# Kernel optimization log

Hardware: AMD Instinct MI355X
Metric: run time of the kernel (lower is better)

Reference implementation:

```python
import jax, jax.numpy as jnp
import numpy as np

N_NODES = 100000
N_EDGES = 1600000
HEADS = 4
HID = 32
NEG_SLOPE = 0.2
EPS = 1e-16


def _gat_layer(x, w, a_src, a_dst, b, src, dst, n_nodes, concat):
    # x: [N, F_in], w: [H*C, F_in], a_src/a_dst: [H, C]
    H, C = a_src.shape
    h = (x @ w.T).reshape(-1, H, C)                      # [N, H, C]
    alpha_src = jnp.einsum('nhc,hc->nh', h, a_src)       # [N, H]
    alpha_dst = jnp.einsum('nhc,hc->nh', h, a_dst)       # [N, H]
    e = alpha_src[src] + alpha_dst[dst]                  # [E, H]
    e = jax.nn.leaky_relu(e, NEG_SLOPE)
    # segment softmax over incoming edges of each dst node
    m = jax.ops.segment_max(e, dst, num_segments=n_nodes)   # [N, H]
    ex = jnp.exp(e - m[dst])
    denom = jax.ops.segment_sum(ex, dst, num_segments=n_nodes)  # [N, H]
    alpha = ex / (denom[dst] + EPS)                      # [E, H]
    msg = alpha[:, :, None] * h[src]                     # [E, H, C]
    out = jax.ops.segment_sum(msg, dst, num_segments=n_nodes)  # [N, H, C]
    if concat:
        out = out.reshape(n_nodes, H * C)
    else:
        out = out.mean(axis=1)
    return out + b


def setup_inputs() -> dict:
    key = jax.random.key(0)
    ks = jax.random.split(key, 16)
    x = jax.random.normal(ks[0], (N_NODES, 3), dtype=jnp.float32)
    edge_index = jax.random.randint(ks[1], (2, N_EDGES), 0, N_NODES, dtype=jnp.int64 if jax.config.read('jax_enable_x64') else jnp.int32)
    s = 0.1
    return {
        'x': x,
        'edge_index': edge_index,
        'w1': jax.random.normal(ks[2], (HEADS * HID, 3)) * s,
        'att_src1': jax.random.normal(ks[3], (HEADS, HID)) * s,
        'att_dst1': jax.random.normal(ks[4], (HEADS, HID)) * s,
        'b1': jax.random.normal(ks[5], (HEADS * HID,)) * s,
        'w2': jax.random.normal(ks[6], (HID, HEADS * HID)) * s,
        'att_src2': jax.random.normal(ks[7], (1, HID)) * s,
        'att_dst2': jax.random.normal(ks[8], (1, HID)) * s,
        'b2': jax.random.normal(ks[9], (HID,)) * s,
        'mlp_w1': jax.random.normal(ks[10], (HID, 2 * HID)) * s,
        'mlp_b1': jax.random.normal(ks[11], (HID,)) * s,
        'mlp_w2': jax.random.normal(ks[12], (1, HID)) * s,
        'mlp_b2': jax.random.normal(ks[13], (1,)) * s,
    }


def reference(x, edge_index, w1, att_src1, att_dst1, b1, w2, att_src2, att_dst2, b2,
              mlp_w1, mlp_b1, mlp_w2, mlp_b2):
    src, dst = edge_index[0], edge_index[1]
    n = x.shape[0]
    # dropout layers are identity in eval mode
    h = _gat_layer(x, w1, att_src1, att_dst1, b1, src, dst, n, concat=True)   # [N, H*C]
    h = jax.nn.elu(h)
    h = _gat_layer(h, w2, att_src2, att_dst2, b2, src, dst, n, concat=False)  # [N, C]
    ef = jnp.concatenate([h[src], h[dst]], axis=-1)                            # [E, 2C]
    ef = jax.nn.relu(ef @ mlp_w1.T + mlp_b1)
    flows = (ef @ mlp_w2.T + mlp_b2).squeeze(-1)                               # [E]
    return jax.nn.relu(flows)
```

## Files before the change

### kernel.cpp

```cpp
#include <hip/hip_runtime.h>
#include <hip/hip_fp16.h>
#include <math.h>

#define N_NODES 100000
#define N_EDGES 1600000
#define NEG_SLOPE 0.2f
#define EPS 1e-16f

#define NBUCK 196
#define CHUNK 4096
#define BLKB 391

typedef _Float16 f16x8 __attribute__((ext_vector_type(8)));
typedef float f32x4 __attribute__((ext_vector_type(4)));

__device__ __forceinline__ float lrelu(float v) { return v > 0.f ? v : NEG_SLOPE * v; }

__device__ __forceinline__ float4 ld4h(const __half* p) {
    uint2 r = *(const uint2*)p;
    __half2 h0 = *reinterpret_cast<const __half2*>(&r.x);
    __half2 h1 = *reinterpret_cast<const __half2*>(&r.y);
    float2 f0 = __half22float2(h0), f1 = __half22float2(h1);
    return make_float4(f0.x, f0.y, f1.x, f1.y);
}

__device__ __forceinline__ void ld8h(const __half* p, float* f) {
    uint4 r = *(const uint4*)p;
    __half2 h0 = *reinterpret_cast<const __half2*>(&r.x);
    __half2 h1 = *reinterpret_cast<const __half2*>(&r.y);
    __half2 h2 = *reinterpret_cast<const __half2*>(&r.z);
    __half2 h3 = *reinterpret_cast<const __half2*>(&r.w);
    float2 f0 = __half22float2(h0), f1 = __half22float2(h1);
    float2 f2 = __half22float2(h2), f3 = __half22float2(h3);
    f[0] = f0.x; f[1] = f0.y; f[2] = f1.x; f[3] = f1.y;
    f[4] = f2.x; f[5] = f2.y; f[6] = f3.x; f[7] = f3.y;
}

__global__ void kA_hist(const int* __restrict__ ei, int* __restrict__ bh) {
    __shared__ int hist[NBUCK];
    int tid = threadIdx.x, b = blockIdx.x;
    if (tid < NBUCK) hist[tid] = 0;
    __syncthreads();
    int base = b * CHUNK;
    #pragma unroll
    for (int i = 0; i < CHUNK / 256; i++) {
        int e = base + i * 256 + tid;
        if (e < N_EDGES) {
            int dst = ei[N_EDGES + e];
            atomicAdd(&hist[dst >> 9], 1);
        }
    }
    __syncthreads();
    if (tid < NBUCK) bh[b * NBUCK + tid] = hist[tid];
}

__global__ void kS1(int* __restrict__ bh, int* __restrict__ bucketStart) {
    __shared__ int tsum[256];
    int k = blockIdx.x, t = threadIdx.x;
    int j0 = 2 * t, j1 = 2 * t + 1;
    int v0 = (j0 < BLKB) ? bh[j0 * NBUCK + k] : 0;
    int v1 = (j1 < BLKB) ? bh[j1 * NBUCK + k] : 0;
    int s = v0 + v1;
    tsum[t] = s;
    __syncthreads();
    for (int off = 1; off < 256; off <<= 1) {
        int tv = (t >= off) ? tsum[t - off] : 0;
        __syncthreads();
        tsum[t] += tv;
        __syncthreads();
    }
    int excl = tsum[t] - s;
    if (j0 < BLKB) bh[j0 * NBUCK + k] = excl;
    if (j1 < BLKB) bh[j1 * NBUCK + k] = excl + v0;
    if (t == 255) bucketStart[k] = tsum[255];
}

__global__ void kS2(int* __restrict__ bucketStart) {
    __shared__ int tmp[256];
    int t = threadIdx.x;
    int v = (t < NBUCK) ? bucketStart[t] : 0;
    tmp[t] = v;
    __syncthreads();
    for (int off = 1; off < 256; off <<= 1) {
        int tv = (t >= off) ? tmp[t - off] : 0;
        __syncthreads();
        tmp[t] += tv;
        __syncthreads();
    }
    if (t < NBUCK) bucketStart[t] = tmp[t] - v;
    if (t == NBUCK - 1) bucketStart[NBUCK] = tmp[t];
}

__global__ void kB_bin(const int* __restrict__ ei, const int* __restrict__ bh,
                       const int* __restrict__ bucketStart, int* __restrict__ binned) {
    __shared__ int cur[NBUCK];
    int tid = threadIdx.x, b = blockIdx.x;
    if (tid < NBUCK) cur[tid] = bucketStart[tid] + bh[b * NBUCK + tid];
    __syncthreads();
    int base = b * CHUNK;
    #pragma unroll
    for (int i = 0; i < CHUNK / 256; i++) {
        int e = base + i * 256 + tid;
        if (e < N_EDGES) {
            int src = ei[e], dst = ei[N_EDGES + e];
            int pos = atomicAdd(&cur[dst >> 9], 1);
            binned[pos] = src | ((dst & 511) << 17);
        }
    }
}

__global__ void kC_sort(const int* __restrict__ bucketStart, const int* __restrict__ binned,
                        int* __restrict__ deg, int* __restrict__ rowptr,
                        int* __restrict__ csr_src) {
    __shared__ int cnt[512];
    __shared__ int pfx[512];
    __shared__ int bsum[256];
    int t = threadIdx.x, k = blockIdx.x;
    int s0 = bucketStart[k], s1 = bucketStart[k + 1];
    cnt[t] = 0; cnt[t + 256] = 0;
    __syncthreads();
    for (int i = s0 + t; i < s1; i += 256)
        atomicAdd(&cnt[binned[i] >> 17], 1);
    __syncthreads();
    int a0 = cnt[2 * t], a1 = cnt[2 * t + 1];
    int s = a0 + a1;
    bsum[t] = s;
    __syncthreads();
    for (int off = 1; off < 256; off <<= 1) {
        int tv = (t >= off) ? bsum[t - off] : 0;
        __syncthreads();
        bsum[t] += tv;
        __syncthreads();
    }
    int excl = bsum[t] - s;
    pfx[2 * t] = excl;
    pfx[2 * t + 1] = excl + a0;
    int nb0 = k << 9;
    int n0 = nb0 + 2 * t, n1 = nb0 + 2 * t + 1;
    if (n0 < N_NODES) { deg[n0] = a0; rowptr[n0] = s0 + excl; }
    if (n1 < N_NODES) { deg[n1] = a1; rowptr[n1] = s0 + excl + a0; }
    __syncthreads();
    for (int i = s0 + t; i < s1; i += 256) {
        int pkd = binned[i];
        int pos = s0 + atomicAdd(&pfx[pkd >> 17], 1);
        csr_src[pos] = pkd & 0x1FFFF;
    }
}

__global__ void k_q(const float* __restrict__ w1, const float* __restrict__ as1,
                    const float* __restrict__ ad1, float* __restrict__ qv) {
    int t = threadIdx.x;
    if (t >= 24) return;
    int c = t % 3, h = (t / 3) % 4, side = t / 12;
    const float* att = side ? ad1 : as1;
    float acc = 0.f;
    for (int cc = 0; cc < 32; cc++)
        acc += att[h * 32 + cc] * w1[(h * 32 + cc) * 3 + c];
    qv[t] = acc;
}

__global__ void k_node1(const float* __restrict__ x, const float* __restrict__ qv,
                        float* __restrict__ a1d, __half* __restrict__ p1h) {
    int n = blockIdx.x * blockDim.x + threadIdx.x;
    if (n >= N_NODES) return;
    float x0 = x[n * 3], x1 = x[n * 3 + 1], x2 = x[n * 3 + 2];
    float s0 = x0 * qv[0]  + x1 * qv[1]  + x2 * qv[2];
    float s1 = x0 * qv[3]  + x1 * qv[4]  + x2 * qv[5];
    float s2 = x0 * qv[6]  + x1 * qv[7]  + x2 * qv[8];
    float s3 = x0 * qv[9]  + x1 * qv[10] + x2 * qv[11];
    float4 d;
    d.x = x0 * qv[12] + x1 * qv[13] + x2 * qv[14];
    d.y = x0 * qv[15] + x1 * qv[16] + x2 * qv[17];
    d.z = x0 * qv[18] + x1 * qv[19] + x2 * qv[20];
    d.w = x0 * qv[21] + x1 * qv[22] + x2 * qv[23];
    ((float4*)a1d)[n] = d;
    __half2 h0 = __floats2half2_rn(s0, s1);
    __half2 h1 = __floats2half2_rn(s2, s3);
    __half2 h2v = __floats2half2_rn(x0, x1);
    __half2 h3 = __floats2half2_rn(x2, 1.f);
    uint4 st;
    st.x = *reinterpret_cast<unsigned int*>(&h0);
    st.y = *reinterpret_cast<unsigned int*>(&h1);
    st.z = *reinterpret_cast<unsigned int*>(&h2v);
    st.w = *reinterpret_cast<unsigned int*>(&h3);
    *reinterpret_cast<uint4*>(p1h + n * 8) = st;
}

#define G1_BLOCKS ((N_NODES + 63) / 64)
__global__ void k_gat1(const int* __restrict__ rowptr, const int* __restrict__ deg,
                       const int* __restrict__ csr_src,
                       const __half* __restrict__ p1h, const float* __restrict__ w1,
                       const float* __restrict__ a1d,
                       const float* __restrict__ b1, const float* __restrict__ w2,
                       const float* __restrict__ as2, const float* __restrict__ ad2,
                       __half* __restrict__ h2, float* __restrict__ a2s, float* __restrict__ a2d) {
    __shared__ float sm[64][16];
    __shared__ __align__(16) __half F1h[4][16][136];
    int tid = threadIdx.x;
    int wave = tid >> 6, lane = tid & 63;

    int nl = wave * 16 + (lane >> 2);
    int h  = lane & 3;
    int n  = blockIdx.x * 64 + nl;
    if (n < N_NODES) {
        float4 ad4 = ((const float4*)a1d)[n];
        float adv[4] = {ad4.x, ad4.y, ad4.z, ad4.w};
        int beg = rowptr[n], cnt = deg[n];
        float acc[4][4];
        #pragma unroll
        for (int hh = 0; hh < 4; hh++)
            acc[hh][0] = acc[hh][1] = acc[hh][2] = acc[hh][3] = 0.f;
        int t = h;
        for (; t + 12 < cnt; t += 16) {
            int i0 = csr_src[beg + t],     i1 = csr_src[beg + t + 4];
            int i2 = csr_src[beg + t + 8], i3 = csr_src[beg + t + 12];
            float g0[8], g1[8], g2[8], g3[8];
            ld8h(p1h + i0 * 8, g0);
            ld8h(p1h + i1 * 8, g1);
            ld8h(p1h + i2 * 8, g2);
            ld8h(p1h + i3 * 8, g3);
            #pragma unroll
            for (int hh = 0; hh < 4; hh++) {
                float e0 = __expf(lrelu(g0[hh] + adv[hh]));
                float e1 = __expf(lrelu(g1[hh] + adv[hh]));
                float e2 = __expf(lrelu(g2[hh] + adv[hh]));
                float e3 = __expf(lrelu(g3[hh] + adv[hh]));
                acc[hh][0] += e0 * g0[4] + e1 * g1[4] + e2 * g2[4] + e3 * g3[4];
                acc[hh][1] += e0 * g0[5] + e1 * g1[5] + e2 * g2[5] + e3 * g3[5];
                acc[hh][2] += e0 * g0[6] + e1 * g1[6] + e2 * g2[6] + e3 * g3[6];
                acc[hh][3] += e0 + e1 + e2 + e3;
            }
        }
        for (; t < cnt; t += 4) {
            int i0 = csr_src[beg + t];
            float g0[8];
            ld8h(p1h + i0 * 8, g0);
            #pragma unroll
            for (int hh = 0; hh < 4; hh++) {
                float e0 = __expf(lrelu(g0[hh] + adv[hh]));
                acc[hh][0] += e0 * g0[4];
                acc[hh][1] += e0 * g0[5];
                acc[hh][2] += e0 * g0[6];
                acc[hh][3] += e0;
            }
        }
        #pragma unroll
        for (int hh = 0; hh < 4; hh++) {
            #pragma unroll
            for (int cc = 0; cc < 4; cc++) {
                float vv = acc[hh][cc];
                vv += __shfl_xor(vv, 1);
                vv += __shfl_xor(vv, 2);
                acc[hh][cc] = vv;
            }
        }
        float4 r;
        r.x = h == 0 ? acc[0][0] : h == 1 ? acc[1][0] : h == 2 ? acc[2][0] : acc[3][0];
        r.y = h == 0 ? acc[0][1] : h == 1 ? acc[1][1] : h == 2 ? acc[2][1] : acc[3][1];
        r.z = h == 0 ? acc[0][2] : h == 1 ? acc[1][2] : h == 2 ? acc[2][2] : acc[3][2];
        r.w = h == 0 ? acc[0][3] : h == 1 ? acc[1][3] : h == 2 ? acc[2][3] : acc[3][3];
        *(float4*)&sm[nl][h * 4] = r;
    }

    f16x8 Bf[2][4];
    {
        int bn = lane & 15, bg = lane >> 4;
        #pragma unroll
        for (int tile = 0; tile < 2; tile++) {
            const float* wrow = w2 + (tile * 16 + bn) * 128 + bg * 8;
            #pragma unroll
            for (int ks = 0; ks < 4; ks++) {
                const float4* wp = (const float4*)(wrow + ks * 32);
                float4 u0 = wp[0], u1 = wp[1];
                f16x8 bf;
                bf[0] = (_Float16)u0.x; bf[1] = (_Float16)u0.y;
                bf[2] = (_Float16)u0.z; bf[3] = (_Float16)u0.w;
                bf[4] = (_Float16)u1.x; bf[5] = (_Float16)u1.y;
                bf[6] = (_Float16)u1.z; bf[7] = (_Float16)u1.w;
                Bf[tile][ks] = bf;
            }
        }
    }

    int j = lane, j2 = lane + 64;
    int h0 = j >> 5;
    float wa0 = w1[j * 3], wa1 = w1[j * 3 + 1], wa2 = w1[j * 3 + 2];
    float wb0 = w1[j2 * 3], wb1 = w1[j2 * 3 + 1], wb2 = w1[j2 * 3 + 2];
    float b1j = b1[j], b1j2 = b1[j2];

    #pragma unroll 1
    for (int i = 0; i < 16; i++) {
        int n2 = blockIdx.x * 64 + wave * 16 + i;
        if (n2 >= N_NODES) break;
        const float* S = sm[wave * 16 + i];
        float v0 = (wa0 * S[h0 * 4] + wa1 * S[h0 * 4 + 1] + wa2 * S[h0 * 4 + 2])
                   / (S[h0 * 4 + 3] + EPS) + b1j;
        float v1 = (wb0 * S[(2 + h0) * 4] + wb1 * S[(2 + h0) * 4 + 1] + wb2 * S[(2 + h0) * 4 + 2])
                   / (S[(2 + h0) * 4 + 3] + EPS) + b1j2;
        float e0 = v0 > 0.f ? v0 : __expf(v0) - 1.f;
        float e1 = v1 > 0.f ? v1 : __expf(v1) - 1.f;
        F1h[wave][i][j]  = __float2half(e0);
        F1h[wave][i][j2] = __float2half(e1);
    }

    f32x4 d0 = {0.f, 0.f, 0.f, 0.f}, d1 = {0.f, 0.f, 0.f, 0.f};
    {
        int am = lane & 15, ag = lane >> 4;
        const __half* Arow = &F1h[wave][am][0];
        #pragma unroll
        for (int ks = 0; ks < 4; ks++) {
            f16x8 af = *(const f16x8*)&Arow[ks * 32 + ag * 8];
            d0 = __builtin_amdgcn_mfma_f32_16x16x32_f16(af, Bf[0][ks], d0, 0, 0, 0);
            d1 = __builtin_amdgcn_mfma_f32_16x16x32_f16(af, Bf[1][ks], d1, 0, 0, 0);
        }
    }

    {
        int ch = lane & 15, rg = lane >> 4;
        float as2a = as2[ch], as2b = as2[ch + 16];
        float ad2a = ad2[ch], ad2b = ad2[ch + 16];
        #pragma unroll
        for (int r = 0; r < 4; r++) {
            int n2 = blockIdx.x * 64 + wave * 16 + rg * 4 + r;
            float va = d0[r], vb = d1[r];
            if (n2 < N_NODES) {
                h2[n2 * 32 + ch]      = __float2half(va);
                h2[n2 * 32 + ch + 16] = __float2half(vb);
            }
            float ps = va * as2a + vb * as2b;
            float pd = va * ad2a + vb * ad2b;
            ps += __shfl_xor(ps, 1); ps += __shfl_xor(ps, 2);
            ps += __shfl_xor(ps, 4); ps += __shfl_xor(ps, 8);
            pd += __shfl_xor(pd, 1); pd += __shfl_xor(pd, 2);
            pd += __shfl_xor(pd, 4); pd += __shfl_xor(pd, 8);
            if (ch == 0 && n2 < N_NODES) { a2s[n2] = ps; a2d[n2] = pd; }
        }
    }
}

#define G2_BLOCKS ((N_NODES + 15) / 16)
__global__ void k_gat2(const int* __restrict__ rowptr, const int* __restrict__ deg,
                       const int* __restrict__ csr_src,
                       const __half* __restrict__ h2, const float* __restrict__ a2s,
                       const float* __restrict__ a2d, const float* __restrict__ b2,
                       const float* __restrict__ mw1, const float* __restrict__ mb1,
                       __half* __restrict__ u, __half* __restrict__ v) {
    __shared__ __align__(16) float WT[32][68];
    __shared__ int   pidx[4][68];
    __shared__ float pe[4][68];
    __shared__ float hfv[4][144];
    int tid = threadIdx.x;
    for (int i = tid; i < 2048; i += 256) {
        int s = i >> 5, k = i & 31;
        WT[k][s] = mw1[(s & 31) * 64 + (s >> 5) * 32 + k];
    }
    __syncthreads();
    int lane = tid & 63, w = tid >> 6;
    int nl = lane >> 4, sl = lane & 15;
    int eg2 = sl >> 2, qq = sl & 3;
    int n = blockIdx.x * 16 + w * 4 + nl;
    float4 b2a = ((const float4*)b2)[qq * 2];
    float4 b2b = ((const float4*)b2)[qq * 2 + 1];

    int beg = 0, cnt = 0;
    float ad = 0.f;
    if (n < N_NODES) { beg = rowptr[n]; cnt = deg[n]; ad = a2d[n]; }

    float acc[8] = {0.f, 0.f, 0.f, 0.f, 0.f, 0.f, 0.f, 0.f};
    float den = 0.f;
    int pkbase = nl * 17;
    for (int b16 = 0; b16 < cnt; b16 += 16) {
        int li = b16 + sl;
        int idx = (li < cnt) ? csr_src[beg + li] : 0;
        float e = 0.f;
        if (li < cnt) e = __expf(lrelu(a2s[idx] + ad));
        den += e;
        pidx[w][pkbase + sl] = idx;
        pe[w][pkbase + sl]   = e;
        #pragma unroll
        for (int p = 0; p < 4; p++) {
            int id = pidx[w][pkbase + p * 4 + eg2];
            float ee = pe[w][pkbase + p * 4 + eg2];
            float g[8];
            ld8h(h2 + id * 32 + qq * 8, g);
            acc[0] += ee * g[0]; acc[1] += ee * g[1];
            acc[2] += ee * g[2]; acc[3] += ee * g[3];
            acc[4] += ee * g[4]; acc[5] += ee * g[5];
            acc[6] += ee * g[6]; acc[7] += ee * g[7];
        }
    }
    #pragma unroll
    for (int j = 0; j < 8; j++) {
        float vv = acc[j];
        vv += __shfl_xor(vv, 4);
        vv += __shfl_xor(vv, 8);
        acc[j] = vv;
    }
    den += __shfl_xor(den, 1); den += __shfl_xor(den, 2);
    den += __shfl_xor(den, 4); den += __shfl_xor(den, 8);
    float inv = 1.f / (den + EPS);
    if (sl < 4) {
        float4 ha, hb;
        ha.x = acc[0] * inv + b2a.x; ha.y = acc[1] * inv + b2a.y;
        ha.z = acc[2] * inv + b2a.z; ha.w = acc[3] * inv + b2a.w;
        hb.x = acc[4] * inv + b2b.x; hb.y = acc[5] * inv + b2b.y;
        hb.z = acc[6] * inv + b2b.z; hb.w = acc[7] * inv + b2b.w;
        *(float4*)&hfv[w][nl * 36 + sl * 8]     = ha;
        *(float4*)&hfv[w][nl * 36 + sl * 8 + 4] = hb;
    }
    if (n < N_NODES) {
        int half_o = sl >> 3, c4 = (sl & 7) * 4;
        __half* outp = half_o ? v : u;
        float r0 = half_o ? 0.f : mb1[c4 + 0];
        float r1 = half_o ? 0.f : mb1[c4 + 1];
        float r2 = half_o ? 0.f : mb1[c4 + 2];
        float r3 = half_o ? 0.f : mb1[c4 + 3];
        const float* hfp = &hfv[w][nl * 36];
        int s4 = sl * 4;
        #pragma unroll
        for (int k = 0; k < 32; k++) {
            float hk = hfp[k];
            float4 wv = *(const float4*)&WT[k][s4];
            r0 += wv.x * hk; r1 += wv.y * hk;
            r2 += wv.z * hk; r3 += wv.w * hk;
        }
        __half2 p0, p1;
        p0.x = __float2half(r0); p0.y = __float2half(r1);
        p1.x = __float2half(r2); p1.y = __float2half(r3);
        uint2 st;
        st.x = *reinterpret_cast<unsigned int*>(&p0);
        st.y = *reinterpret_cast<unsigned int*>(&p1);
        *reinterpret_cast<uint2*>(outp + n * 32 + c4) = st;
    }
}

#define MLP_BLOCKS 4096
__global__ void k_mlp(const int* __restrict__ ei, const __half* __restrict__ u,
                      const __half* __restrict__ v, const float* __restrict__ mw2,
                      const float* __restrict__ mb2, float* __restrict__ out) {
    int tid = threadIdx.x;
    int q = tid & 7;
    float4 w2q = ((const float4*)mw2)[q];
    float mb20 = mb2[0];
    int g = blockIdx.x * 32 + (tid >> 3);
    const int stride = MLP_BLOCKS * 32 * 4;
    for (int e = g * 4; e < N_EDGES; e += stride) {
        int eb = e;
        int e1 = (eb + 1 < N_EDGES) ? eb + 1 : eb;
        int e2 = (eb + 2 < N_EDGES) ? eb + 2 : eb;
        int e3 = (eb + 3 < N_EDGES) ? eb + 3 : eb;
        int sa = ei[eb], da = ei[N_EDGES + eb];
        int sb = ei[e1], db = ei[N_EDGES + e1];
        int sc = ei[e2], dc = ei[N_EDGES + e2];
        int sd = ei[e3], dd = ei[N_EDGES + e3];
        float4 ua = ld4h(u + sa * 32 + q * 4);
        float4 va = ld4h(v + da * 32 + q * 4);
        float4 ub = ld4h(u + sb * 32 + q * 4);
        float4 vb = ld4h(v + db * 32 + q * 4);
        float4 uc = ld4h(u + sc * 32 + q * 4);
        float4 vc = ld4h(v + dc * 32 + q * 4);
        float4 ud = ld4h(u + sd * 32 + q * 4);
        float4 vd = ld4h(v + dd * 32 + q * 4);
        float s0 = fmaxf(ua.x + va.x, 0.f) * w2q.x + fmaxf(ua.y + va.y, 0.f) * w2q.y
                 + fmaxf(ua.z + va.z, 0.f) * w2q.z + fmaxf(ua.w + va.w, 0.f) * w2q.w;
        float s1 = fmaxf(ub.x + vb.x, 0.f) * w2q.x + fmaxf(ub.y + vb.y, 0.f) * w2q.y
                 + fmaxf(ub.z + vb.z, 0.f) * w2q.z + fmaxf(ub.w + vb.w, 0.f) * w2q.w;
        float s2 = fmaxf(uc.x + vc.x, 0.f) * w2q.x + fmaxf(uc.y + vc.y, 0.f) * w2q.y
                 + fmaxf(uc.z + vc.z, 0.f) * w2q.z + fmaxf(uc.w + vc.w, 0.f) * w2q.w;
        float s3 = fmaxf(ud.x + vd.x, 0.f) * w2q.x + fmaxf(ud.y + vd.y, 0.f) * w2q.y
                 + fmaxf(ud.z + vd.z, 0.f) * w2q.z + fmaxf(ud.w + vd.w, 0.f) * w2q.w;
        s0 += __shfl_xor(s0, 1, 8); s0 += __shfl_xor(s0, 2, 8); s0 += __shfl_xor(s0, 4, 8);
        s1 += __shfl_xor(s1, 1, 8); s1 += __shfl_xor(s1, 2, 8); s1 += __shfl_xor(s1, 4, 8);
        s2 += __shfl_xor(s2, 1, 8); s2 += __shfl_xor(s2, 2, 8); s2 += __shfl_xor(s2, 4, 8);
        s3 += __shfl_xor(s3, 1, 8); s3 += __shfl_xor(s3, 2, 8); s3 += __shfl_xor(s3, 4, 8);
        if (q == 0) {
            out[eb] = fmaxf(s0 + mb20, 0.f);
            if (eb + 1 < N_EDGES) out[eb + 1] = fmaxf(s1 + mb20, 0.f);
            if (eb + 2 < N_EDGES) out[eb + 2] = fmaxf(s2 + mb20, 0.f);
            if (eb + 3 < N_EDGES) out[eb + 3] = fmaxf(s3 + mb20, 0.f);
        }
    }
}

extern "C" void kernel_launch(void* const* d_in, const int* in_sizes, int n_in,
                              void* d_out, int out_size, void* d_ws, size_t ws_size,
                              hipStream_t stream) {
    const float* x    = (const float*)d_in[0];
    const int*   ei   = (const int*)d_in[1];
    const float* w1   = (const float*)d_in[2];
    const float* as1  = (const float*)d_in[3];
    const float* ad1  = (const float*)d_in[4];
    const float* b1   = (const float*)d_in[5];
    const float* w2   = (const float*)d_in[6];
    const float* as2  = (const float*)d_in[7];
    const float* ad2  = (const float*)d_in[8];
    const float* b2   = (const float*)d_in[9];
    const float* mw1  = (const float*)d_in[10];
    const float* mb1  = (const float*)d_in[11];
    const float* mw2  = (const float*)d_in[12];
    const float* mb2  = (const float*)d_in[13];
    float* out = (float*)d_out;

    const int N = N_NODES;
    char* base   = (char*)d_ws;
    int* deg     = (int*)(base);
    int* rowptr  = (int*)(base + 400000);
    int* bstart  = (int*)(base + 800000);
    int* bh      = (int*)(base + 1200000);
    int* csr_src = (int*)(base + 1602048);
    __half* p1h  = (__half*)(base + 8002048);
    float* a1d   = (float*)(base + 11202048);
    __half* h2   = (__half*)(base + 12802048);
    int* binned  = (int*)(base + 19202048);
    float* a2s   = (float*)(base + 25602048);
    float* a2d   = (float*)(base + 26002048);
    __half* u    = (__half*)(base + 26402048);
    __half* v    = (__half*)(base + 32802048);
    float* qv    = (float*)(base + 39202048);

    const int nb = (N + 255) / 256;

    kA_hist<<<BLKB, 256, 0, stream>>>(ei, bh);
    kS1<<<NBUCK, 256, 0, stream>>>(bh, bstart);
    kS2<<<1, 256, 0, stream>>>(bstart);
    kB_bin<<<BLKB, 256, 0, stream>>>(ei, bh, bstart, binned);
    kC_sort<<<NBUCK, 256, 0, stream>>>(bstart, binned, deg, rowptr, csr_src);

    k_q<<<1, 32, 0, stream>>>(w1, as1, ad1, qv);
    k_node1<<<nb, 256, 0, stream>>>(x, qv, a1d, p1h);

    k_gat1<<<G1_BLOCKS, 256, 0, stream>>>(rowptr, deg, csr_src, p1h, w1, a1d,
                                          b1, w2, as2, ad2, h2, a2s, a2d);

    k_gat2<<<G2_BLOCKS, 256, 0, stream>>>(rowptr, deg, csr_src, h2, a2s, a2d, b2,
                                          mw1, mb1, u, v);

    k_mlp<<<MLP_BLOCKS, 256, 0, stream>>>(ei, u, v, mw2, mb2, out);
}
```

Baseline: 245.2 us.

## Fuse node projection into histogram, fold bucket scan into consumers, cache bucket in LDS

Merges the attention-projection precompute and per-node layer-1 kernel into the edge histogram kernel. The single-block bucket prefix scan is dropped and recomputed redundantly inside the binning and sort kernels. The sort kernel stages each bucket's edges in shared memory so the second pass reads from LDS rather than global memory. This removes three kernel launches and one global pass, at the cost of redundant scans and about 36KB more LDS per sort block, which may reduce occupancy.

```diff
diff --git a/kernel.cpp b/kernel.cpp
--- a/kernel.cpp
+++ b/kernel.cpp
@@ -10,6 +10,7 @@
 #define NBUCK 196
 #define CHUNK 4096
 #define BLKB 391
+#define EBUF_CAP 9216
 
 typedef _Float16 f16x8 __attribute__((ext_vector_type(8)));
 typedef float f32x4 __attribute__((ext_vector_type(4)));
@@ -36,11 +37,48 @@
     f[4] = f2.x; f[5] = f2.y; f[6] = f3.x; f[7] = f3.y;
 }
 
-__global__ void kA_hist(const int* __restrict__ ei, int* __restrict__ bh) {
+__global__ void kA_hist_node(const int* __restrict__ ei, int* __restrict__ bh,
+                             const float* __restrict__ x, const float* __restrict__ w1,
+                             const float* __restrict__ as1, const float* __restrict__ ad1,
+                             float* __restrict__ a1d, __half* __restrict__ p1h) {
     __shared__ int hist[NBUCK];
+    __shared__ float qvs[24];
     int tid = threadIdx.x, b = blockIdx.x;
     if (tid < NBUCK) hist[tid] = 0;
-    __syncthreads();
+    if (tid >= 224 && tid < 248) {
+        int t = tid - 224;
+        int c = t % 3, h = (t / 3) % 4, side = t / 12;
+        const float* att = side ? ad1 : as1;
+        float acc = 0.f;
+        for (int cc = 0; cc < 32; cc++)
+            acc += att[h * 32 + cc] * w1[(h * 32 + cc) * 3 + c];
+        qvs[t] = acc;
+    }
+    __syncthreads();
+    int n = b * 256 + tid;
+    if (n < N_NODES) {
+        float x0 = x[n * 3], x1 = x[n * 3 + 1], x2 = x[n * 3 + 2];
+        float s0 = x0 * qvs[0]  + x1 * qvs[1]  + x2 * qvs[2];
+        float s1 = x0 * qvs[3]  + x1 * qvs[4]  + x2 * qvs[5];
+        float s2 = x0 * qvs[6]  + x1 * qvs[7]  + x2 * qvs[8];
+        float s3 = x0 * qvs[9]  + x1 * qvs[10] + x2 * qvs[11];
+        float4 d;
+        d.x = x0 * qvs[12] + x1 * qvs[13] + x2 * qvs[14];
+        d.y = x0 * qvs[15] + x1 * qvs[16] + x2 * qvs[17];
+        d.z = x0 * qvs[18] + x1 * qvs[19] + x2 * qvs[20];
+        d.w = x0 * qvs[21] + x1 * qvs[22] + x2 * qvs[23];
+        ((float4*)a1d)[n] = d;
+        __half2 h0 = __floats2half2_rn(s0, s1);
+        __half2 h1 = __floats2half2_rn(s2, s3);
+        __half2 h2v = __floats2half2_rn(x0, x1);
+        __half2 h3 = __floats2half2_rn(x2, 1.f);
+        uint4 st;
+        st.x = *reinterpret_cast<unsigned int*>(&h0);
+        st.y = *reinterpret_cast<unsigned int*>(&h1);
+        st.z = *reinterpret_cast<unsigned int*>(&h2v);
+        st.w = *reinterpret_cast<unsigned int*>(&h3);
+        *reinterpret_cast<uint4*>(p1h + n * 8) = st;
+    }
     int base = b * CHUNK;
     #pragma unroll
     for (int i = 0; i < CHUNK / 256; i++) {
@@ -54,7 +92,7 @@
     if (tid < NBUCK) bh[b * NBUCK + tid] = hist[tid];
 }
 
-__global__ void kS1(int* __restrict__ bh, int* __restrict__ bucketStart) {
+__global__ void kS1(int* __restrict__ bh, int* __restrict__ bucketTot) {
     __shared__ int tsum[256];
     int k = blockIdx.x, t = threadIdx.x;
     int j0 = 2 * t, j1 = 2 * t + 1;
@@ -72,30 +110,24 @@
     int excl = tsum[t] - s;
     if (j0 < BLKB) bh[j0 * NBUCK + k] = excl;
     if (j1 < BLKB) bh[j1 * NBUCK + k] = excl + v0;
-    if (t == 255) bucketStart[k] = tsum[255];
-}
-
-__global__ void kS2(int* __restrict__ bucketStart) {
+    if (t == 255) bucketTot[k] = tsum[255];
+}
+
+__global__ void kB_bin(const int* __restrict__ ei, const int* __restrict__ bh,
+                       const int* __restrict__ bucketTot, int* __restrict__ binned) {
+    __shared__ int cur[NBUCK];
     __shared__ int tmp[256];
-    int t = threadIdx.x;
-    int v = (t < NBUCK) ? bucketStart[t] : 0;
-    tmp[t] = v;
+    int tid = threadIdx.x, b = blockIdx.x;
+    int v = (tid < NBUCK) ? bucketTot[tid] : 0;
+    tmp[tid] = v;
     __syncthreads();
     for (int off = 1; off < 256; off <<= 1) {
-        int tv = (t >= off) ? tmp[t - off] : 0;
-        __syncthreads();
-        tmp[t] += tv;
-        __syncthreads();
-    }
-    if (t < NBUCK) bucketStart[t] = tmp[t] - v;
-    if (t == NBUCK - 1) bucketStart[NBUCK] = tmp[t];
-}
-
-__global__ void kB_bin(const int* __restrict__ ei, const int* __restrict__ bh,
-                       const int* __restrict__ bucketStart, int* __restrict__ binned) {
-    __shared__ int cur[NBUCK];
-    int tid = threadIdx.x, b = blockIdx.x;
-    if (tid < NBUCK) cur[tid] = bucketStart[tid] + bh[b * NBUCK + tid];
+        int tv = (tid >= off) ? tmp[tid - off] : 0;
+        __syncthreads();
+        tmp[tid] += tv;
+        __syncthreads();
+    }
+    if (tid < NBUCK) cur[tid] = (tmp[tid] - v) + bh[b * NBUCK + tid];
     __syncthreads();
     int base = b * CHUNK;
     #pragma unroll
@@ -109,18 +141,40 @@
     }
 }
 
-__global__ void kC_sort(const int* __restrict__ bucketStart, const int* __restrict__ binned,
+__global__ void kC_sort(const int* __restrict__ bucketTot, const int* __restrict__ binned,
                         int* __restrict__ deg, int* __restrict__ rowptr,
                         int* __restrict__ csr_src) {
+    __shared__ int ebuf[EBUF_CAP];
     __shared__ int cnt[512];
     __shared__ int pfx[512];
     __shared__ int bsum[256];
+    __shared__ int tmp[256];
     int t = threadIdx.x, k = blockIdx.x;
-    int s0 = bucketStart[k], s1 = bucketStart[k + 1];
+    int v = (t < NBUCK) ? bucketTot[t] : 0;
+    tmp[t] = v;
+    __syncthreads();
+    for (int off = 1; off < 256; off <<= 1) {
+        int tv = (t >= off) ? tmp[t - off] : 0;
+        __syncthreads();
+        tmp[t] += tv;
+        __syncthreads();
+    }
+    int tot = bucketTot[k];
+    int s0 = tmp[k] - tot, s1 = s0 + tot;
     cnt[t] = 0; cnt[t + 256] = 0;
     __syncthreads();
-    for (int i = s0 + t; i < s1; i += 256)
-        atomicAdd(&cnt[binned[i] >> 17], 1);
+    int m = s1 - s0;
+    bool inl = (m <= EBUF_CAP);
+    if (inl) {
+        for (int i = t; i < m; i += 256) {
+            int pkd = binned[s0 + i];
+            ebuf[i] = pkd;
+            atomicAdd(&cnt[pkd >> 17], 1);
+        }
+    } else {
+        for (int i = s0 + t; i < s1; i += 256)
+            atomicAdd(&cnt[binned[i] >> 17], 1);
+    }
     __syncthreads();
     int a0 = cnt[2 * t], a1 = cnt[2 * t + 1];
     int s = a0 + a1;
@@ -140,50 +194,19 @@
     if (n0 < N_NODES) { deg[n0] = a0; rowptr[n0] = s0 + excl; }
     if (n1 < N_NODES) { deg[n1] = a1; rowptr[n1] = s0 + excl + a0; }
     __syncthreads();
-    for (int i = s0 + t; i < s1; i += 256) {
-        int pkd = binned[i];
-        int pos = s0 + atomicAdd(&pfx[pkd >> 17], 1);
-        csr_src[pos] = pkd & 0x1FFFF;
-    }
-}
-
-__global__ void k_q(const float* __restrict__ w1, const float* __restrict__ as1,
-                    const float* __restrict__ ad1, float* __restrict__ qv) {
-    int t = threadIdx.x;
-    if (t >= 24) return;
-    int c = t % 3, h = (t / 3) % 4, side = t / 12;
-    const float* att = side ? ad1 : as1;
-    float acc = 0.f;
-    for (int cc = 0; cc < 32; cc++)
-        acc += att[h * 32 + cc] * w1[(h * 32 + cc) * 3 + c];
-    qv[t] = acc;
-}
-
-__global__ void k_node1(const float* __restrict__ x, const float* __restrict__ qv,
-                        float* __restrict__ a1d, __half* __restrict__ p1h) {
-    int n = blockIdx.x * blockDim.x + threadIdx.x;
-    if (n >= N_NODES) return;
-    float x0 = x[n * 3], x1 = x[n * 3 + 1], x2 = x[n * 3 + 2];
-    float s0 = x0 * qv[0]  + x1 * qv[1]  + x2 * qv[2];
-    float s1 = x0 * qv[3]  + x1 * qv[4]  + x2 * qv[5];
-    float s2 = x0 * qv[6]  + x1 * qv[7]  + x2 * qv[8];
-    float s3 = x0 * qv[9]  + x1 * qv[10] + x2 * qv[11];
-    float4 d;
-    d.x = x0 * qv[12] + x1 * qv[13] + x2 * qv[14];
-    d.y = x0 * qv[15] + x1 * qv[16] + x2 * qv[17];
-    d.z = x0 * qv[18] + x1 * qv[19] + x2 * qv[20];
-    d.w = x0 * qv[21] + x1 * qv[22] + x2 * qv[23];
-    ((float4*)a1d)[n] = d;
-    __half2 h0 = __floats2half2_rn(s0, s1);
-    __half2 h1 = __floats2half2_rn(s2, s3);
-    __half2 h2v = __floats2half2_rn(x0, x1);
-    __half2 h3 = __floats2half2_rn(x2, 1.f);
-    uint4 st;
-    st.x = *reinterpret_cast<unsigned int*>(&h0);
-    st.y = *reinterpret_cast<unsigned int*>(&h1);
-    st.z = *reinterpret_cast<unsigned int*>(&h2v);
-    st.w = *reinterpret_cast<unsigned int*>(&h3);
-    *reinterpret_cast<uint4*>(p1h + n * 8) = st;
+    if (inl) {
+        for (int i = t; i < m; i += 256) {
+            int pkd = ebuf[i];
+            int pos = s0 + atomicAdd(&pfx[pkd >> 17], 1);
+            csr_src[pos] = pkd & 0x1FFFF;
+        }
+    } else {
+        for (int i = s0 + t; i < s1; i += 256) {
+            int pkd = binned[i];
+            int pos = s0 + atomicAdd(&pfx[pkd >> 17], 1);
+            csr_src[pos] = pkd & 0x1FFFF;
+        }
+    }
 }
 
 #define G1_BLOCKS ((N_NODES + 63) / 64)
@@ -501,11 +524,10 @@
     const float* mb2  = (const float*)d_in[13];
     float* out = (float*)d_out;
 
-    const int N = N_NODES;
     char* base   = (char*)d_ws;
     int* deg     = (int*)(base);
     int* rowptr  = (int*)(base + 400000);
-    int* bstart  = (int*)(base + 800000);
+    int* btot    = (int*)(base + 800000);
     int* bh      = (int*)(base + 1200000);
     int* csr_src = (int*)(base + 1602048);
     __half* p1h  = (__half*)(base + 8002048);
@@ -516,18 +538,11 @@
     float* a2d   = (float*)(base + 26002048);
     __half* u    = (__half*)(base + 26402048);
     __half* v    = (__half*)(base + 32802048);
-    float* qv    = (float*)(base + 39202048);
-
-    const int nb = (N + 255) / 256;
-
-    kA_hist<<<BLKB, 256, 0, stream>>>(ei, bh);
-    kS1<<<NBUCK, 256, 0, stream>>>(bh, bstart);
-    kS2<<<1, 256, 0, stream>>>(bstart);
-    kB_bin<<<BLKB, 256, 0, stream>>>(ei, bh, bstart, binned);
-    kC_sort<<<NBUCK, 256, 0, stream>>>(bstart, binned, deg, rowptr, csr_src);
-
-    k_q<<<1, 32, 0, stream>>>(w1, as1, ad1, qv);
-    k_node1<<<nb, 256, 0, stream>>>(x, qv, a1d, p1h);
+
+    kA_hist_node<<<BLKB, 256, 0, stream>>>(ei, bh, x, w1, as1, ad1, a1d, p1h);
+    kS1<<<NBUCK, 256, 0, stream>>>(bh, btot);
+    kB_bin<<<BLKB, 256, 0, stream>>>(ei, bh, btot, binned);
+    kC_sort<<<NBUCK, 256, 0, stream>>>(btot, binned, deg, rowptr, csr_src);
 
     k_gat1<<<G1_BLOCKS, 256, 0, stream>>>(rowptr, deg, csr_src, p1h, w1, a1d,
                                           b1, w2, as2, ad2, h2, a2s, a2d);
```

Result: faster. 239.1 us (median of 2 runs) (-2.5%).
